# Kernel optimization log

Hardware: AMD Instinct MI355X
Metric: run time of the kernel (lower is better)

Reference implementation:

```python
import jax, jax.numpy as jnp
import numpy as np

ATTN = 128

def _gelu(x):
    return jax.nn.gelu(x, approximate=False)

def _mlp3(x, W1, b1, W2, b2, W3, b3):
    h = _gelu(x @ W1.T + b1)
    h = _gelu(h @ W2.T + b2)
    return h @ W3.T + b3

def setup_inputs() -> dict:
    key = jax.random.key(0)
    ks = jax.random.split(key, 32)
    B, K, M, C = 128, 64, 2048, 32
    QD, AD, H = 128, 128, 256
    s = 0.02
    d = {}
    d['g'] = jax.random.normal(ks[0], (B, K, 3), dtype=jnp.float32)
    d['query'] = jax.random.normal(ks[1], (M, QD), dtype=jnp.float32) * s
    d['qW'] = jax.random.normal(ks[2], (AD, QD), dtype=jnp.float32) * s
    d['qb'] = jnp.zeros((AD,), jnp.float32)
    d['kW'] = jax.random.normal(ks[3], (AD, 1), dtype=jnp.float32) * s
    d['kb'] = jnp.zeros((AD,), jnp.float32)
    # global_mlp: K -> H -> H -> H
    d['gm_W1'] = jax.random.normal(ks[4], (H, K), dtype=jnp.float32) * s
    d['gm_b1'] = jnp.zeros((H,), jnp.float32)
    d['gm_W2'] = jax.random.normal(ks[5], (H, H), dtype=jnp.float32) * s
    d['gm_b2'] = jnp.zeros((H,), jnp.float32)
    d['gm_W3'] = jax.random.normal(ks[6], (H, H), dtype=jnp.float32) * s
    d['gm_b3'] = jnp.zeros((H,), jnp.float32)
    # point_mlp: (H+QD+1) -> H -> H -> H
    d['pm_W1'] = jax.random.normal(ks[7], (H, H + QD + 1), dtype=jnp.float32) * s
    d['pm_b1'] = jnp.zeros((H,), jnp.float32)
    d['pm_W2'] = jax.random.normal(ks[8], (H, H), dtype=jnp.float32) * s
    d['pm_b2'] = jnp.zeros((H,), jnp.float32)
    d['pm_W3'] = jax.random.normal(ks[9], (H, H), dtype=jnp.float32) * s
    d['pm_b3'] = jnp.zeros((H,), jnp.float32)
    d['tW'] = jax.random.normal(ks[10], (C, H), dtype=jnp.float32) * s
    d['tb'] = jnp.zeros((C,), jnp.float32)
    d['wW'] = jax.random.normal(ks[11], (1, H), dtype=jnp.float32) * s
    d['wb'] = jnp.zeros((1,), jnp.float32)
    d['cW'] = jax.random.normal(ks[12], (1, H), dtype=jnp.float32) * s
    d['cb'] = jnp.zeros((1,), jnp.float32)
    return d

def reference(g, query, qW, qb, kW, kb,
              gm_W1, gm_b1, gm_W2, gm_b2, gm_W3, gm_b3,
              pm_W1, pm_b1, pm_W2, pm_b2, pm_W3, pm_b3,
              tW, tb, wW, wb, cW, cb):
    B, K, _ = g.shape
    M = query.shape[0]
    inv = jnp.linalg.norm(g, axis=-1)                    # (B,K)
    Q = query @ qW.T + qb                                # (M,AD)
    Kk = inv[..., None] * kW[:, 0] + kb                  # (B,K,AD) Linear(1->AD)
    scores = jnp.einsum('md,bkd->bmk', Q, Kk) / jnp.sqrt(jnp.float32(Q.shape[-1]))
    A = jax.nn.softmax(scores, axis=-1)                  # (B,M,K)
    y = jnp.einsum('bmk,bkd->bmd', A, g)                 # (B,M,3)
    global_s = _mlp3(inv, gm_W1, gm_b1, gm_W2, gm_b2, gm_W3, gm_b3)  # (B,H)
    attended_inv = jnp.einsum('bmk,bk->bm', A, inv)      # (B,M)
    s_in = jnp.concatenate([
        jnp.broadcast_to(global_s[:, None, :], (B, M, global_s.shape[-1])),
        jnp.broadcast_to(query[None], (B, M, query.shape[-1])),
        attended_inv[..., None],
    ], axis=-1)                                          # (B,M,H+QD+1)
    s = _mlp3(s_in, pm_W1, pm_b1, pm_W2, pm_b2, pm_W3, pm_b3)  # (B,M,H)
    type_logits = s @ tW.T + tb                          # (B,M,C)
    weight_logits = (s @ wW.T + wb)[..., 0]              # (B,M)
    gate = jnp.clip(jax.nn.sigmoid(s @ cW.T + cb), 0.0, 1.0)  # (B,M,1)
    y = y * gate
    return (y, type_logits, weight_logits)
```

## Files before the change

### kernel.cpp

```cpp
#include <hip/hip_runtime.h>
#include <hip/hip_bf16.h>
#include <math.h>


typedef __attribute__((ext_vector_type(8))) short short8;
typedef __attribute__((ext_vector_type(4))) float f32x4;
typedef __attribute__((ext_vector_type(16))) float f32x16;

__device__ __forceinline__ unsigned short bf16_rne(float f){
    union { float f; unsigned u; } v; v.f = f;
    return (unsigned short)((v.u + 0x7FFFu + ((v.u >> 16) & 1u)) >> 16);
}
__device__ __forceinline__ unsigned pk_bf16(float a, float b){
    float2 t; t.x = a; t.y = b;
    __hip_bfloat162 h = __float22bfloat162_rn(t);
    union { __hip_bfloat162 h; unsigned u; } cv; cv.h = h;
    return cv.u;
}
__device__ __forceinline__ short8 cvt8_f4(const float* __restrict__ p){
    float4 a = *(const float4*)p;
    float4 b = *(const float4*)(p + 4);
    short8 s;
    s[0]=(short)bf16_rne(a.x); s[1]=(short)bf16_rne(a.y);
    s[2]=(short)bf16_rne(a.z); s[3]=(short)bf16_rne(a.w);
    s[4]=(short)bf16_rne(b.x); s[5]=(short)bf16_rne(b.y);
    s[6]=(short)bf16_rne(b.z); s[7]=(short)bf16_rne(b.w);
    return s;
}

__device__ __forceinline__ float gelu_f(float x){
    float z  = x * 0.70710678118654752f;
    float az = fabsf(z);
    float t  = __builtin_amdgcn_rcpf(1.0f + 0.3275911f * az);
    float p  = t*(0.254829592f + t*(-0.284496736f + t*(1.421413741f + t*(-1.453152027f + t*1.061405429f))));
    float e  = __expf(-az*az);
    float er = copysignf(1.0f - p*e, z);
    return 0.5f * x * (1.0f + er);
}
__device__ __forceinline__ float gelu_poly(float x){
    float t = x*x;
    float p = fmaf(t, -2.9761905e-3f, 2.5e-2f);
    p = fmaf(t, p, -0.16666667f);
    p = fmaf(t, p, 1.0f);
    float Phi = fmaf(x*p, 0.39894228f, 0.5f);
    Phi = fminf(fmaxf(Phi, 0.0f), 1.0f);
    return x * Phi;
}

__global__ __launch_bounds__(256)
void k_prep(const float* __restrict__ g, const float* __restrict__ qW,
            const float* __restrict__ qb, const float* __restrict__ kW,
            const float* __restrict__ query, const float* __restrict__ pmW1,
            const float* __restrict__ pmb1,
            const float* __restrict__ pmW2, const float* __restrict__ pmW3,
            const float* __restrict__ pmb3,
            const float* __restrict__ gmW1, const float* __restrict__ gmb1,
            const float* __restrict__ gmW2, const float* __restrict__ gmb2,
            const float* __restrict__ gmW3, const float* __restrict__ gmb3,
            const float* __restrict__ tW, const float* __restrict__ tb,
            const float* __restrict__ wW, const float* __restrict__ wb,
            const float* __restrict__ cW, const float* __restrict__ cb,
            float* __restrict__ invg, float* __restrict__ ag,
            float* __restrict__ u1g, float* __restrict__ u2g,
            unsigned short* __restrict__ w2b, unsigned short* __restrict__ wheadb,
            float* __restrict__ bheadg, float* __restrict__ w385g) {
    __shared__ __align__(16) unsigned char smem[87040];
    const int bid = blockIdx.x, tid = threadIdx.x;
    const int w = tid >> 6, lane = tid & 63, q = lane >> 4, ln = lane & 15;

    if (bid < 32) {
        int idx = bid*256 + tid;
        const float* p = g + idx*3;
        invg[idx] = sqrtf(p[0]*p[0] + p[1]*p[1] + p[2]*p[2]);
    } else if (bid < 96) {
        int o = (bid - 32)*1024 + tid*4;
        float4 x = *(const float4*)&pmW2[o];
        union { unsigned short u[4]; uint2 v; } r;
        r.u[0] = bf16_rne(x.x); r.u[1] = bf16_rne(x.y);
        r.u[2] = bf16_rne(x.z); r.u[3] = bf16_rne(x.w);
        *(uint2*)&w2b[o] = r.v;
    } else if (bid < 130) {
        float* hw = (float*)smem;
        int c = bid - 96;
        const float* src = (c < 32) ? (tW + c*256) : ((c == 32) ? wW : cW);
        hw[tid] = src[tid];
        __syncthreads();
        float acc = 0.f;
        for (int j = 0; j < 256; ++j) acc += hw[j] * pmW3[j*256 + tid];
        wheadb[c*256 + tid] = bf16_rne(acc);
        if (tid == 0) {
            float bacc = (c < 32) ? tb[c] : ((c == 32) ? wb[0] : cb[0]);
            for (int j = 0; j < 256; ++j) bacc += hw[j] * pmb3[j];
            bheadg[c] = bacc;
        }
    } else if (bid == 130) {
        w385g[tid] = pmW1[tid*385 + 384];
    } else if (bid < 139) {
        float* kws = (float*)smem;
        float* vs  = kws + 128;
        float* red = vs  + 128;
        if (tid < 128) kws[tid] = kW[tid];
        __syncthreads();
        if (tid < 128) {
            float acc = 0.f;
            for (int d = 0; d < 128; ++d) acc += qW[d*128 + tid] * kws[d];
            vs[tid] = acc;
            red[tid] = qb[tid] * kws[tid];
        }
        __syncthreads();
        float s0 = 0.f;
        #pragma unroll 8
        for (int i = 0; i < 128; ++i) s0 += red[i];
        int m = (bid - 131)*256 + tid;
        const float4* qp = (const float4*)(query + m*128);
        float acc = s0;
        #pragma unroll 8
        for (int e4 = 0; e4 < 32; ++e4) {
            float4 qv = qp[e4];
            acc += qv.x*vs[e4*4] + qv.y*vs[e4*4+1] + qv.z*vs[e4*4+2] + qv.w*vs[e4*4+3];
        }
        ag[m] = acc * 0.08838834764831845f;
    } else if (bid < 141) {
        unsigned short* invA = (unsigned short*)smem;
        unsigned short* hA   = (unsigned short*)(smem + 9216);
        unsigned short* hB   = (unsigned short*)(smem + 43008);
        const int b0 = (bid - 139)*64;
        for (int i = tid; i < 4096; i += 256) {
            int r = i >> 6, k = i & 63;
            const float* p = g + ((size_t)(b0 + r)*64 + k)*3;
            invA[r*72 + k] = bf16_rne(sqrtf(p[0]*p[0] + p[1]*p[1] + p[2]*p[2]));
        }
        __syncthreads();

        f32x4 acc[4][4];
        #pragma unroll
        for (int mt = 0; mt < 4; ++mt)
            #pragma unroll
            for (int nt = 0; nt < 4; ++nt) acc[mt][nt] = (f32x4){0.f,0.f,0.f,0.f};
        #pragma unroll
        for (int kk = 0; kk < 2; ++kk) {
            const int kc = kk*32 + q*8;
            short8 af[4], bf_[4];
            #pragma unroll
            for (int mt = 0; mt < 4; ++mt) af[mt] = *(const short8*)&invA[(mt*16 + ln)*72 + kc];
            #pragma unroll
            for (int nt = 0; nt < 4; ++nt) bf_[nt] = cvt8_f4(gmW1 + (w*64 + nt*16 + ln)*64 + kc);
            #pragma unroll
            for (int mt = 0; mt < 4; ++mt)
                #pragma unroll
                for (int nt = 0; nt < 4; ++nt)
                    acc[mt][nt] = __builtin_amdgcn_mfma_f32_16x16x32_bf16(af[mt], bf_[nt], acc[mt][nt], 0, 0, 0);
        }
        #pragma unroll
        for (int mt = 0; mt < 4; ++mt)
            #pragma unroll
            for (int nt = 0; nt < 4; ++nt) {
                const int n = w*64 + nt*16 + ln;
                const float bb = gmb1[n];
                #pragma unroll
                for (int rg = 0; rg < 4; ++rg)
                    hA[(mt*16 + q*4 + rg)*264 + n] = bf16_rne(gelu_f(acc[mt][nt][rg] + bb));
            }
        __syncthreads();
        #pragma unroll
        for (int mt = 0; mt < 4; ++mt)
            #pragma unroll
            for (int nt = 0; nt < 4; ++nt) acc[mt][nt] = (f32x4){0.f,0.f,0.f,0.f};
        for (int kk = 0; kk < 8; ++kk) {
            const int kc = kk*32 + q*8;
            short8 af[4], bf_[4];
            #pragma unroll
            for (int mt = 0; mt < 4; ++mt) af[mt] = *(const short8*)&hA[(mt*16 + ln)*264 + kc];
            #pragma unroll
            for (int nt = 0; nt < 4; ++nt) bf_[nt] = cvt8_f4(gmW2 + (w*64 + nt*16 + ln)*256 + kc);
            #pragma unroll
            for (int mt = 0; mt < 4; ++mt)
                #pragma unroll
                for (int nt = 0; nt < 4; ++nt)
                    acc[mt][nt] = __builtin_amdgcn_mfma_f32_16x16x32_bf16(af[mt], bf_[nt], acc[mt][nt], 0, 0, 0);
        }
        __syncthreads();
        #pragma unroll
        for (int mt = 0; mt < 4; ++mt)
            #pragma unroll
            for (int nt = 0; nt < 4; ++nt) {
                const int n = w*64 + nt*16 + ln;
                const float bb = gmb2[n];
                #pragma unroll
                for (int rg = 0; rg < 4; ++rg)
                    hB[(mt*16 + q*4 + rg)*264 + n] = bf16_rne(gelu_f(acc[mt][nt][rg] + bb));
            }
        __syncthreads();
        #pragma unroll
        for (int mt = 0; mt < 4; ++mt)
            #pragma unroll
            for (int nt = 0; nt < 4; ++nt) acc[mt][nt] = (f32x4){0.f,0.f,0.f,0.f};
        for (int kk = 0; kk < 8; ++kk) {
            const int kc = kk*32 + q*8;
            short8 af[4], bf_[4];
            #pragma unroll
            for (int mt = 0; mt < 4; ++mt) af[mt] = *(const short8*)&hB[(mt*16 + ln)*264 + kc];
            #pragma unroll
            for (int nt = 0; nt < 4; ++nt) bf_[nt] = cvt8_f4(gmW3 + (w*64 + nt*16 + ln)*256 + kc);
            #pragma unroll
            for (int mt = 0; mt < 4; ++mt)
                #pragma unroll
                for (int nt = 0; nt < 4; ++nt)
                    acc[mt][nt] = __builtin_amdgcn_mfma_f32_16x16x32_bf16(af[mt], bf_[nt], acc[mt][nt], 0, 0, 0);
        }
        __syncthreads();
        #pragma unroll
        for (int mt = 0; mt < 4; ++mt)
            #pragma unroll
            for (int nt = 0; nt < 4; ++nt) {
                const int n = w*64 + nt*16 + ln;
                const float bb = gmb3[n];
                #pragma unroll
                for (int rg = 0; rg < 4; ++rg)
                    hA[(mt*16 + q*4 + rg)*264 + n] = bf16_rne(acc[mt][nt][rg] + bb);
            }
        unsigned short* w1s = (unsigned short*)(smem + 43008);
        #pragma unroll
        for (int mt = 0; mt < 4; ++mt)
            #pragma unroll
            for (int nt = 0; nt < 4; ++nt) acc[mt][nt] = (f32x4){0.f,0.f,0.f,0.f};
        for (int chunk = 0; chunk < 4; ++chunk) {
            __syncthreads();
            for (int i = tid; i < 256*64; i += 256) {
                int n = i >> 6, c = i & 63;
                w1s[n*72 + c] = bf16_rne(pmW1[(size_t)n*385 + chunk*64 + c]);
            }
            __syncthreads();
            #pragma unroll
            for (int kk2 = 0; kk2 < 2; ++kk2) {
                const int kl = kk2*32 + q*8;
                const int kg = chunk*64 + kl;
                short8 af[4], bf_[4];
                #pragma unroll
                for (int mt = 0; mt < 4; ++mt) af[mt] = *(const short8*)&hA[(mt*16 + ln)*264 + kg];
                #pragma unroll
                for (int nt = 0; nt < 4; ++nt) bf_[nt] = *(const short8*)&w1s[(w*64 + nt*16 + ln)*72 + kl];
                #pragma unroll
                for (int mt = 0; mt < 4; ++mt)
                    #pragma unroll
                    for (int nt = 0; nt < 4; ++nt)
                        acc[mt][nt] = __builtin_amdgcn_mfma_f32_16x16x32_bf16(af[mt], bf_[nt], acc[mt][nt], 0, 0, 0);
            }
        }
        #pragma unroll
        for (int mt = 0; mt < 4; ++mt)
            #pragma unroll
            for (int nt = 0; nt < 4; ++nt) {
                const int n = w*64 + nt*16 + ln;
                const float bb = pmb1[n];
                #pragma unroll
                for (int rg = 0; rg < 4; ++rg)
                    u1g[(size_t)(b0 + mt*16 + q*4 + rg)*256 + n] = acc[mt][nt][rg] + bb;
            }
    } else {
        unsigned short* qs = (unsigned short*)smem;
        unsigned short* wsd = (unsigned short*)(smem + 17408);
        const int m0 = (bid - 141)*64;
        for (int i = tid; i < 64*128; i += 256) {
            int r = i >> 7, c = i & 127;
            qs[r*136 + c] = bf16_rne(query[(size_t)(m0 + r)*128 + c]);
        }
        for (int i = tid; i < 256*128; i += 256) {
            int n = i >> 7, c = i & 127;
            wsd[n*136 + c] = bf16_rne(pmW1[(size_t)n*385 + 256 + c]);
        }
        __syncthreads();
        f32x4 acc[4][4];
        #pragma unroll
        for (int mt = 0; mt < 4; ++mt)
            #pragma unroll
            for (int nt = 0; nt < 4; ++nt) acc[mt][nt] = (f32x4){0.f,0.f,0.f,0.f};
        #pragma unroll
        for (int kk = 0; kk < 4; ++kk) {
            const int kc = kk*32 + q*8;
            short8 af[4], bf_[4];
            #pragma unroll
            for (int mt = 0; mt < 4; ++mt) af[mt] = *(const short8*)&qs[(mt*16 + ln)*136 + kc];
            #pragma unroll
            for (int nt = 0; nt < 4; ++nt) bf_[nt] = *(const short8*)&wsd[(w*64 + nt*16 + ln)*136 + kc];
            #pragma unroll
            for (int mt = 0; mt < 4; ++mt)
                #pragma unroll
                for (int nt = 0; nt < 4; ++nt)
                    acc[mt][nt] = __builtin_amdgcn_mfma_f32_16x16x32_bf16(af[mt], bf_[nt], acc[mt][nt], 0, 0, 0);
        }
        #pragma unroll
        for (int mt = 0; mt < 4; ++mt)
            #pragma unroll
            for (int nt = 0; nt < 4; ++nt) {
                const int n = w*64 + nt*16 + ln;
                #pragma unroll
                for (int rg = 0; rg < 4; ++rg)
                    u2g[(size_t)(m0 + mt*16 + q*4 + rg)*256 + n] = acc[mt][nt][rg];
            }
    }
}

__global__ __launch_bounds__(256, 4)
void k_main(const float* __restrict__ g,
            const float* __restrict__ invg, const float* __restrict__ ag,
            const float* __restrict__ u1g, const float* __restrict__ u2g,
            const float* __restrict__ w385g, const float* __restrict__ pmb2,
            const unsigned short* __restrict__ w2b, const unsigned short* __restrict__ wheadb,
            const float* __restrict__ bheadg, float* __restrict__ out) {
    __shared__ __align__(16) unsigned short hb[64*264];
    __shared__ __align__(16) float u1s[256], w385s[256], pmb2s[256];
    __shared__ float invs[64], gsl[192], ainv_s[64], y0s[192];

    const int tid = threadIdx.x;
    const int bid = blockIdx.x;
    const int b  = bid >> 5;
    const int m0 = (bid & 31) << 6;

    if (tid < 64)  invs[tid] = invg[b*64 + tid];
    if (tid < 192) gsl[tid]  = g[b*192 + tid];
    u1s[tid]   = u1g[b*256 + tid];
    w385s[tid] = w385g[tid];
    pmb2s[tid] = pmb2[tid];
    __syncthreads();

    {
        const int r = tid >> 2, sub = tid & 3;
        const float am = ag[m0 + r];
        const int kb = sub * 16;
        float mx = -1e30f;
        #pragma unroll
        for (int i = 0; i < 16; ++i) mx = fmaxf(mx, invs[kb + i] * am);
        #pragma unroll
        for (int d = 1; d < 4; d <<= 1) mx = fmaxf(mx, __shfl_xor(mx, d, 64));
        float den = 0.f, ai = 0.f, y0 = 0.f, y1 = 0.f, y2 = 0.f;
        #pragma unroll
        for (int i = 0; i < 16; ++i) {
            const int k = kb + i;
            const float iv = invs[k];
            const float e = __expf(iv * am - mx);
            den += e; ai += e * iv;
            y0 += e * gsl[k*3+0]; y1 += e * gsl[k*3+1]; y2 += e * gsl[k*3+2];
        }
        #pragma unroll
        for (int d = 1; d < 4; d <<= 1) {
            den += __shfl_xor(den, d, 64);
            ai  += __shfl_xor(ai , d, 64);
            y0  += __shfl_xor(y0 , d, 64);
            y1  += __shfl_xor(y1 , d, 64);
            y2  += __shfl_xor(y2 , d, 64);
        }
        if (sub == 0) {
            const float id = 1.0f / den;
            ainv_s[r] = ai * id;
            y0s[r*3+0] = y0*id; y0s[r*3+1] = y1*id; y0s[r*3+2] = y2*id;
        }
    }
    __syncthreads();

    const int w = tid >> 6, lane = tid & 63;
    const int q = lane >> 4, ln = lane & 15;
    const int h5 = lane >> 5, m31 = lane & 31;

    const unsigned short* w2p = w2b + (size_t)(w*64 + m31)*256 + h5*8;
    short8 acur0 = *(const short8*)(w2p);
    short8 acur1 = *(const short8*)(w2p + 32*256);

    {
        const int ln16 = tid & 15, rbase = tid >> 4;
        #pragma unroll
        for (int rr = 0; rr < 4; ++rr) {
            const int r = rr*16 + rbase;
            const float aiv = ainv_s[r];
            const float* u2p = u2g + (size_t)(m0 + r)*256;
            #pragma unroll
            for (int k = 0; k < 4; ++k) {
                const int c = ln16*4 + k*64;
                float4 x  = *(const float4*)&u2p[c];
                float4 uv = *(const float4*)&u1s[c];
                float4 wv = *(const float4*)&w385s[c];
                float g0 = gelu_poly(x.x + uv.x + aiv*wv.x);
                float g1 = gelu_poly(x.y + uv.y + aiv*wv.y);
                float g2 = gelu_poly(x.z + uv.z + aiv*wv.z);
                float g3 = gelu_poly(x.w + uv.w + aiv*wv.w);
                uint2 pk; pk.x = pk_bf16(g0, g1); pk.y = pk_bf16(g2, g3);
                *(uint2*)&hb[r*264 + c] = pk;
            }
        }
    }
    __syncthreads();

    f32x16 acc2[2][2];
    #pragma unroll
    for (int a = 0; a < 2; ++a)
        #pragma unroll
        for (int c = 0; c < 2; ++c)
            #pragma unroll
            for (int i = 0; i < 16; ++i) acc2[a][c][i] = 0.f;

    {
        short8 anxt0, anxt1;
        #pragma unroll
        for (int kk = 0; kk < 16; ++kk) {
            if (kk < 15) {
                anxt0 = *(const short8*)(w2p + (kk+1)*16);
                anxt1 = *(const short8*)(w2p + 32*256 + (kk+1)*16);
            }
            const int kc = kk*16 + h5*8;
            short8 b0 = *(const short8*)&hb[(m31     )*264 + kc];
            short8 b1 = *(const short8*)&hb[(32 + m31)*264 + kc];
            acc2[0][0] = __builtin_amdgcn_mfma_f32_32x32x16_bf16(acur0, b0, acc2[0][0], 0, 0, 0);
            acc2[0][1] = __builtin_amdgcn_mfma_f32_32x32x16_bf16(acur0, b1, acc2[0][1], 0, 0, 0);
            acc2[1][0] = __builtin_amdgcn_mfma_f32_32x32x16_bf16(acur1, b0, acc2[1][0], 0, 0, 0);
            acc2[1][1] = __builtin_amdgcn_mfma_f32_32x32x16_bf16(acur1, b1, acc2[1][1], 0, 0, 0);
            acur0 = anxt0; acur1 = anxt1;
        }
    }
    __syncthreads();

    #pragma unroll
    for (int a = 0; a < 2; ++a) {
        #pragma unroll
        for (int gg = 0; gg < 4; ++gg) {
            const int n0 = w*64 + a*32 + gg*8 + h5*4;
            const float4 bb4 = *(const float4*)&pmb2s[n0];
            #pragma unroll
            for (int c = 0; c < 2; ++c) {
                const int m = c*32 + m31;
                float h0 = gelu_poly(acc2[a][c][gg*4+0] + bb4.x);
                float h1 = gelu_poly(acc2[a][c][gg*4+1] + bb4.y);
                float h2 = gelu_poly(acc2[a][c][gg*4+2] + bb4.z);
                float h3 = gelu_poly(acc2[a][c][gg*4+3] + bb4.w);
                uint2 pk2; pk2.x = pk_bf16(h0, h1); pk2.y = pk_bf16(h2, h3);
                *(uint2*)&hb[m*264 + n0] = pk2;
            }
        }
    }

    const int cb2 = (ln < 2) ? (32 + ln) : 33;
    const unsigned short* whp = wheadb + q*8;
    short8 wf0 = *(const short8*)(whp +  ln      *256);
    short8 wf1 = *(const short8*)(whp + (16 + ln)*256);
    short8 wf2 = *(const short8*)(whp +  cb2     *256);
    __syncthreads();

    f32x4 accA0 = {0.f,0.f,0.f,0.f}, accA1 = {0.f,0.f,0.f,0.f}, accB = {0.f,0.f,0.f,0.f};
    const int rr = w*16 + ln;
    #pragma unroll
    for (int kk = 0; kk < 8; ++kk) {
        short8 wn0, wn1, wn2;
        if (kk < 7) {
            wn0 = *(const short8*)(whp +  ln      *256 + (kk+1)*32);
            wn1 = *(const short8*)(whp + (16 + ln)*256 + (kk+1)*32);
            wn2 = *(const short8*)(whp +  cb2     *256 + (kk+1)*32);
        }
        short8 bh = *(const short8*)&hb[rr*264 + kk*32 + q*8];
        accA0 = __builtin_amdgcn_mfma_f32_16x16x32_bf16(wf0, bh, accA0, 0, 0, 0);
        accA1 = __builtin_amdgcn_mfma_f32_16x16x32_bf16(wf1, bh, accA1, 0, 0, 0);
        accB  = __builtin_amdgcn_mfma_f32_16x16x32_bf16(wf2, bh, accB , 0, 0, 0);
        wf0 = wn0; wf1 = wn1; wf2 = wn2;
    }
    {
        const size_t row = (size_t)b*2048 + m0 + rr;
        const int c0 = q*4;
        f32x4 r0 = accA0 + *(const f32x4*)&bheadg[c0];
        f32x4 r1 = accA1 + *(const f32x4*)&bheadg[16 + c0];
        *(f32x4*)&out[786432 + row*32 + c0]      = r0;
        *(f32x4*)&out[786432 + row*32 + 16 + c0] = r1;
        if (q == 0) {
            out[9175040 + row] = accB[0] + bheadg[32];
            float gv = accB[1] + bheadg[33];
            float gt = 1.0f / (1.0f + __expf(-gv));
            gt = fminf(fmaxf(gt, 0.0f), 1.0f);
            float* yo = out + row*3;
            yo[0] = y0s[rr*3+0] * gt;
            yo[1] = y0s[rr*3+1] * gt;
            yo[2] = y0s[rr*3+2] * gt;
        }
    }
}

extern "C" void kernel_launch(void* const* d_in, const int* in_sizes, int n_in,
                              void* d_out, int out_size, void* d_ws, size_t ws_size,
                              hipStream_t stream) {
    const float* g     = (const float*)d_in[0];
    const float* query = (const float*)d_in[1];
    const float* qW    = (const float*)d_in[2];
    const float* qb    = (const float*)d_in[3];
    const float* kW    = (const float*)d_in[4];
    const float* gmW1  = (const float*)d_in[6];
    const float* gmb1  = (const float*)d_in[7];
    const float* gmW2  = (const float*)d_in[8];
    const float* gmb2  = (const float*)d_in[9];
    const float* gmW3  = (const float*)d_in[10];
    const float* gmb3  = (const float*)d_in[11];
    const float* pmW1  = (const float*)d_in[12];
    const float* pmb1  = (const float*)d_in[13];
    const float* pmW2  = (const float*)d_in[14];
    const float* pmb2  = (const float*)d_in[15];
    const float* pmW3  = (const float*)d_in[16];
    const float* pmb3  = (const float*)d_in[17];
    const float* tW    = (const float*)d_in[18];
    const float* tb    = (const float*)d_in[19];
    const float* wW    = (const float*)d_in[20];
    const float* wb    = (const float*)d_in[21];
    const float* cW    = (const float*)d_in[22];
    const float* cb    = (const float*)d_in[23];
    float* out = (float*)d_out;

    float* ws    = (float*)d_ws;
    float* invg  = ws;
    float* ag    = ws + 8192;
    float* u1g   = ws + 10240;
    float* w385g = ws + 43008;
    float* bheadg= ws + 43264;
    unsigned short* w2b    = (unsigned short*)(ws + 43328);
    unsigned short* wheadb = (unsigned short*)(ws + 76096);
    float* u2g   = ws + 80448;

    hipLaunchKernelGGL(k_prep, dim3(173), dim3(256), 0, stream,
                       g, qW, qb, kW, query, pmW1, pmb1, pmW2, pmW3, pmb3,
                       gmW1, gmb1, gmW2, gmb2, gmW3, gmb3,
                       tW, tb, wW, wb, cW, cb,
                       invg, ag, u1g, u2g, w2b, wheadb, bheadg, w385g);
    hipLaunchKernelGGL(k_main, dim3(4096), dim3(256), 0, stream,
                       g, invg, ag, u1g, u2g, w385g, pmb2,
                       w2b, wheadb, bheadg, out);
}
```

Baseline: 259.8 us.

## Halve k_main row tile to 32 and split head MFMAs across wave pairs

Each k_main block now handles 32 query rows instead of 64, which halves the LDS hidden buffer and the layer-2 accumulators. The launch bound rises to 6 blocks per CU and the grid doubles to 8192 blocks. In the head stage, even waves compute the type logits and odd waves compute the weight/gate logits for the same 16 rows. The aim is higher occupancy and less register pressure. The cost is that each w2 weight fragment loaded from global memory is now reused across half as many rows, so weight traffic per row doubles.

```diff
diff --git a/kernel.cpp b/kernel.cpp
--- a/kernel.cpp
+++ b/kernel.cpp
@@ -301,21 +301,21 @@
     }
 }
 
-__global__ __launch_bounds__(256, 4)
+__global__ __launch_bounds__(256, 6)
 void k_main(const float* __restrict__ g,
             const float* __restrict__ invg, const float* __restrict__ ag,
             const float* __restrict__ u1g, const float* __restrict__ u2g,
             const float* __restrict__ w385g, const float* __restrict__ pmb2,
             const unsigned short* __restrict__ w2b, const unsigned short* __restrict__ wheadb,
             const float* __restrict__ bheadg, float* __restrict__ out) {
-    __shared__ __align__(16) unsigned short hb[64*264];
+    __shared__ __align__(16) unsigned short hb[32*264];
     __shared__ __align__(16) float u1s[256], w385s[256], pmb2s[256];
-    __shared__ float invs[64], gsl[192], ainv_s[64], y0s[192];
+    __shared__ float invs[64], gsl[192], ainv_s[32], y0s[96];
 
     const int tid = threadIdx.x;
     const int bid = blockIdx.x;
-    const int b  = bid >> 5;
-    const int m0 = (bid & 31) << 6;
+    const int b  = bid >> 6;
+    const int m0 = (bid & 63) << 5;
 
     if (tid < 64)  invs[tid] = invg[b*64 + tid];
     if (tid < 192) gsl[tid]  = g[b*192 + tid];
@@ -325,17 +325,17 @@
     __syncthreads();
 
     {
-        const int r = tid >> 2, sub = tid & 3;
+        const int r = tid >> 3, sub = tid & 7;
         const float am = ag[m0 + r];
-        const int kb = sub * 16;
+        const int kb = sub * 8;
         float mx = -1e30f;
         #pragma unroll
-        for (int i = 0; i < 16; ++i) mx = fmaxf(mx, invs[kb + i] * am);
-        #pragma unroll
-        for (int d = 1; d < 4; d <<= 1) mx = fmaxf(mx, __shfl_xor(mx, d, 64));
+        for (int i = 0; i < 8; ++i) mx = fmaxf(mx, invs[kb + i] * am);
+        #pragma unroll
+        for (int d = 1; d < 8; d <<= 1) mx = fmaxf(mx, __shfl_xor(mx, d, 64));
         float den = 0.f, ai = 0.f, y0 = 0.f, y1 = 0.f, y2 = 0.f;
         #pragma unroll
-        for (int i = 0; i < 16; ++i) {
+        for (int i = 0; i < 8; ++i) {
             const int k = kb + i;
             const float iv = invs[k];
             const float e = __expf(iv * am - mx);
@@ -343,7 +343,7 @@
             y0 += e * gsl[k*3+0]; y1 += e * gsl[k*3+1]; y2 += e * gsl[k*3+2];
         }
         #pragma unroll
-        for (int d = 1; d < 4; d <<= 1) {
+        for (int d = 1; d < 8; d <<= 1) {
             den += __shfl_xor(den, d, 64);
             ai  += __shfl_xor(ai , d, 64);
             y0  += __shfl_xor(y0 , d, 64);
@@ -369,7 +369,7 @@
     {
         const int ln16 = tid & 15, rbase = tid >> 4;
         #pragma unroll
-        for (int rr = 0; rr < 4; ++rr) {
+        for (int rr = 0; rr < 2; ++rr) {
             const int r = rr*16 + rbase;
             const float aiv = ainv_s[r];
             const float* u2p = u2g + (size_t)(m0 + r)*256;
@@ -390,13 +390,11 @@
     }
     __syncthreads();
 
-    f32x16 acc2[2][2];
+    f32x16 acc2[2];
     #pragma unroll
     for (int a = 0; a < 2; ++a)
         #pragma unroll
-        for (int c = 0; c < 2; ++c)
-            #pragma unroll
-            for (int i = 0; i < 16; ++i) acc2[a][c][i] = 0.f;
+        for (int i = 0; i < 16; ++i) acc2[a][i] = 0.f;
 
     {
         short8 anxt0, anxt1;
@@ -407,12 +405,9 @@
                 anxt1 = *(const short8*)(w2p + 32*256 + (kk+1)*16);
             }
             const int kc = kk*16 + h5*8;
-            short8 b0 = *(const short8*)&hb[(m31     )*264 + kc];
-            short8 b1 = *(const short8*)&hb[(32 + m31)*264 + kc];
-            acc2[0][0] = __builtin_amdgcn_mfma_f32_32x32x16_bf16(acur0, b0, acc2[0][0], 0, 0, 0);
-            acc2[0][1] = __builtin_amdgcn_mfma_f32_32x32x16_bf16(acur0, b1, acc2[0][1], 0, 0, 0);
-            acc2[1][0] = __builtin_amdgcn_mfma_f32_32x32x16_bf16(acur1, b0, acc2[1][0], 0, 0, 0);
-            acc2[1][1] = __builtin_amdgcn_mfma_f32_32x32x16_bf16(acur1, b1, acc2[1][1], 0, 0, 0);
+            short8 b0 = *(const short8*)&hb[m31*264 + kc];
+            acc2[0] = __builtin_amdgcn_mfma_f32_32x32x16_bf16(acur0, b0, acc2[0], 0, 0, 0);
+            acc2[1] = __builtin_amdgcn_mfma_f32_32x32x16_bf16(acur1, b0, acc2[1], 0, 0, 0);
             acur0 = anxt0; acur1 = anxt1;
         }
     }
@@ -424,50 +419,59 @@
         for (int gg = 0; gg < 4; ++gg) {
             const int n0 = w*64 + a*32 + gg*8 + h5*4;
             const float4 bb4 = *(const float4*)&pmb2s[n0];
-            #pragma unroll
-            for (int c = 0; c < 2; ++c) {
-                const int m = c*32 + m31;
-                float h0 = gelu_poly(acc2[a][c][gg*4+0] + bb4.x);
-                float h1 = gelu_poly(acc2[a][c][gg*4+1] + bb4.y);
-                float h2 = gelu_poly(acc2[a][c][gg*4+2] + bb4.z);
-                float h3 = gelu_poly(acc2[a][c][gg*4+3] + bb4.w);
-                uint2 pk2; pk2.x = pk_bf16(h0, h1); pk2.y = pk_bf16(h2, h3);
-                *(uint2*)&hb[m*264 + n0] = pk2;
-            }
+            float h0 = gelu_poly(acc2[a][gg*4+0] + bb4.x);
+            float h1 = gelu_poly(acc2[a][gg*4+1] + bb4.y);
+            float h2 = gelu_poly(acc2[a][gg*4+2] + bb4.z);
+            float h3 = gelu_poly(acc2[a][gg*4+3] + bb4.w);
+            uint2 pk2; pk2.x = pk_bf16(h0, h1); pk2.y = pk_bf16(h2, h3);
+            *(uint2*)&hb[m31*264 + n0] = pk2;
         }
     }
 
     const int cb2 = (ln < 2) ? (32 + ln) : 33;
     const unsigned short* whp = wheadb + q*8;
-    short8 wf0 = *(const short8*)(whp +  ln      *256);
-    short8 wf1 = *(const short8*)(whp + (16 + ln)*256);
-    short8 wf2 = *(const short8*)(whp +  cb2     *256);
+    const bool evenw = ((w & 1) == 0);
+    short8 wf0, wf1, wf2;
+    if (evenw) {
+        wf0 = *(const short8*)(whp +  ln      *256);
+        wf1 = *(const short8*)(whp + (16 + ln)*256);
+    } else {
+        wf2 = *(const short8*)(whp +  cb2     *256);
+    }
     __syncthreads();
 
+    const int rr = (w >> 1)*16 + ln;
     f32x4 accA0 = {0.f,0.f,0.f,0.f}, accA1 = {0.f,0.f,0.f,0.f}, accB = {0.f,0.f,0.f,0.f};
-    const int rr = w*16 + ln;
     #pragma unroll
     for (int kk = 0; kk < 8; ++kk) {
         short8 wn0, wn1, wn2;
         if (kk < 7) {
-            wn0 = *(const short8*)(whp +  ln      *256 + (kk+1)*32);
-            wn1 = *(const short8*)(whp + (16 + ln)*256 + (kk+1)*32);
-            wn2 = *(const short8*)(whp +  cb2     *256 + (kk+1)*32);
+            if (evenw) {
+                wn0 = *(const short8*)(whp +  ln      *256 + (kk+1)*32);
+                wn1 = *(const short8*)(whp + (16 + ln)*256 + (kk+1)*32);
+            } else {
+                wn2 = *(const short8*)(whp +  cb2     *256 + (kk+1)*32);
+            }
         }
         short8 bh = *(const short8*)&hb[rr*264 + kk*32 + q*8];
-        accA0 = __builtin_amdgcn_mfma_f32_16x16x32_bf16(wf0, bh, accA0, 0, 0, 0);
-        accA1 = __builtin_amdgcn_mfma_f32_16x16x32_bf16(wf1, bh, accA1, 0, 0, 0);
-        accB  = __builtin_amdgcn_mfma_f32_16x16x32_bf16(wf2, bh, accB , 0, 0, 0);
-        wf0 = wn0; wf1 = wn1; wf2 = wn2;
+        if (evenw) {
+            accA0 = __builtin_amdgcn_mfma_f32_16x16x32_bf16(wf0, bh, accA0, 0, 0, 0);
+            accA1 = __builtin_amdgcn_mfma_f32_16x16x32_bf16(wf1, bh, accA1, 0, 0, 0);
+            wf0 = wn0; wf1 = wn1;
+        } else {
+            accB  = __builtin_amdgcn_mfma_f32_16x16x32_bf16(wf2, bh, accB , 0, 0, 0);
+            wf2 = wn2;
+        }
     }
     {
         const size_t row = (size_t)b*2048 + m0 + rr;
         const int c0 = q*4;
-        f32x4 r0 = accA0 + *(const f32x4*)&bheadg[c0];
-        f32x4 r1 = accA1 + *(const f32x4*)&bheadg[16 + c0];
-        *(f32x4*)&out[786432 + row*32 + c0]      = r0;
-        *(f32x4*)&out[786432 + row*32 + 16 + c0] = r1;
-        if (q == 0) {
+        if (evenw) {
+            f32x4 r0 = accA0 + *(const f32x4*)&bheadg[c0];
+            f32x4 r1 = accA1 + *(const f32x4*)&bheadg[16 + c0];
+            *(f32x4*)&out[786432 + row*32 + c0]      = r0;
+            *(f32x4*)&out[786432 + row*32 + 16 + c0] = r1;
+        } else if (q == 0) {
             out[9175040 + row] = accB[0] + bheadg[32];
             float gv = accB[1] + bheadg[33];
             float gt = 1.0f / (1.0f + __expf(-gv));
@@ -523,7 +527,7 @@
                        gmW1, gmb1, gmW2, gmb2, gmW3, gmb3,
                        tW, tb, wW, wb, cW, cb,
                        invg, ag, u1g, u2g, w2b, wheadb, bheadg, w385g);
-    hipLaunchKernelGGL(k_main, dim3(4096), dim3(256), 0, stream,
+    hipLaunchKernelGGL(k_main, dim3(8192), dim3(256), 0, stream,
                        g, invg, ag, u1g, u2g, w385g, pmb2,
                        w2b, wheadb, bheadg, out);
 }
```

Result: slower. 314.9 us (+21.2%).
